# Kernel tuning notes

Measured on AMD Instinct MI355X. Metric: run time of the kernel, lower is better.

The kernel has to match this reference:

```python
import jax, jax.numpy as jnp
import numpy as np

V = 4          # view_num
B = 2048       # batch_size
D = 512        # feature dim
N = V * B
TEMP = 0.5     # temperature
EPS = 1e-8     # torch CosineSimilarity eps


def _neg_idx():
    # Row with residue p (position within its view block) masks out columns c
    # with c % B == p (the positive/self positions), exactly matching
    # mask_positive_samples: fill_diagonal_(0) on every BxB block.
    cols = np.arange(N)
    return np.stack([cols[cols % B != p] for p in range(B)])  # [B, N-V]

_NEG_IDX = jnp.asarray(_neg_idx())


def setup_inputs() -> dict:
    key = jax.random.key(0)
    x = jax.random.normal(key, (V, B, D), dtype=jnp.float32)
    return {"x": x}


def reference(x):
    # torch.cat(input, dim=0) -> [N, D]
    xf = x.reshape(N, D)
    # Cosine similarity via normalize + matmul (same math as broadcasted
    # CosineSimilarity(dim=2), expressed efficiently).
    norm = jnp.maximum(jnp.linalg.norm(xf, axis=1, keepdims=True), EPS)
    xn = xf / norm
    sim = (xn @ xn.T) / TEMP                                  # [N, N]

    # Negatives per anchor row: gather masked columns (same column order as
    # torch boolean-mask indexing, which is row-major ascending).
    sim_v = sim.reshape(V, B, N)
    negs = jnp.take_along_axis(sim_v, _NEG_IDX[None], axis=2)  # [V, B, N-V]
    lse_neg = jax.nn.logsumexp(negs, axis=2)                   # [V, B]

    # pos[i, j, b] = sim block-diagonal between views i and j
    pos = jnp.diagonal(sim.reshape(V, B, V, B), axis1=1, axis2=3)  # [V, V, B]

    # CrossEntropy with label 0 on logits = [pos_ij, negatives_i]:
    #   loss_b = logsumexp([pos, negs]) - pos = logaddexp(pos, lse_neg) - pos
    lse = jnp.logaddexp(pos, lse_neg[:, None, :])              # [V, V, B]
    per_pair = (lse - pos).sum(axis=2) / B                     # [V, V]

    off_diag = 1.0 - jnp.eye(V, dtype=per_pair.dtype)          # skip j == i
    return jnp.sum(per_pair * off_diag)
```

## Files before the change

kernel.cpp:

```cpp
#include <hip/hip_runtime.h>
#include <hip/hip_fp8.h>

#define NV 4
#define NB 2048
#define ND 512
#define NN 8192

typedef int int8v __attribute__((ext_vector_type(8)));
typedef int int4v __attribute__((ext_vector_type(4)));
typedef float floatx4 __attribute__((ext_vector_type(4)));
#define SCALE1 0x7F7F7F7Fu

__device__ __forceinline__ void lds_barrier() {
  asm volatile("s_waitcnt lgkmcnt(0)\n\ts_barrier" ::: "memory");
}

__global__ __launch_bounds__(256) void normalize_k(const float* __restrict__ x,
                                                   unsigned char* __restrict__ xn,
                                                   float* __restrict__ sumexp,
                                                   float* __restrict__ out) {
  if (threadIdx.x < 4) sumexp[blockIdx.x * 4 + threadIdx.x] = 0.0f;
  if (blockIdx.x == 0 && threadIdx.x == 0) out[0] = 0.0f;

  const int row = blockIdx.x * 4 + (threadIdx.x >> 6);
  const int l = threadIdx.x & 63;
  const float4* xr = (const float4*)(x + (size_t)row * ND);
  float4 v0 = xr[l * 2 + 0];
  float4 v1 = xr[l * 2 + 1];
  float ss = v0.x * v0.x + v0.y * v0.y + v0.z * v0.z + v0.w * v0.w +
             v1.x * v1.x + v1.y * v1.y + v1.z * v1.z + v1.w * v1.w;
#pragma unroll
  for (int off = 32; off > 0; off >>= 1) ss += __shfl_xor(ss, off, 64);
  const float inv = 1.0f / fmaxf(sqrtf(ss), 1e-8f);
  union { unsigned char b[8]; uint2 u; } pk;
  pk.b[0] = __hip_fp8_e4m3(v0.x * inv).__x;
  pk.b[1] = __hip_fp8_e4m3(v0.y * inv).__x;
  pk.b[2] = __hip_fp8_e4m3(v0.z * inv).__x;
  pk.b[3] = __hip_fp8_e4m3(v0.w * inv).__x;
  pk.b[4] = __hip_fp8_e4m3(v1.x * inv).__x;
  pk.b[5] = __hip_fp8_e4m3(v1.y * inv).__x;
  pk.b[6] = __hip_fp8_e4m3(v1.z * inv).__x;
  pk.b[7] = __hip_fp8_e4m3(v1.w * inv).__x;
  *(uint2*)(xn + (size_t)row * ND + l * 8) = pk.u;
}

__global__ __launch_bounds__(256) void sim_k(const unsigned char* __restrict__ xn,
                                             float* __restrict__ sumexp,
                                             float* __restrict__ pos) {
  __shared__ unsigned char As[128 * 128];
  __shared__ unsigned char Bs[128 * 128];
  const int tid = threadIdx.x;
  const int l = tid & 63;
  const int m = l & 15, q = l >> 4, s = l & 7;
  const int wr = (tid >> 6) >> 1, wc = (tid >> 6) & 1;

  const int bid = blockIdx.x;
  int rt = (int)((129.0f - sqrtf(16641.0f - 8.0f * (float)bid)) * 0.5f);
  rt = rt < 0 ? 0 : (rt > 63 ? 63 : rt);
  while (rt > 0 && (rt * 64 - rt * (rt - 1) / 2) > bid) --rt;
  while (rt < 63 && ((rt + 1) * 64 - (rt + 1) * rt / 2) <= bid) ++rt;
  const int ct = rt + (bid - (rt * 64 - rt * (rt - 1) / 2));
  const bool diag = (rt == ct);

  floatx4 acc[4][4] = {};

  const unsigned char* gA = xn + (size_t)rt * 128 * ND;
  const unsigned char* gB = xn + (size_t)ct * 128 * ND;

  const int crow = tid >> 3;
  const int coff = (tid & 7) * 16;
  const int lsw = ((tid & 7) ^ ((tid >> 3) & 7)) * 16;

  const int fo0 = ((2 * q + 0) ^ s) * 16;
  const int fo1 = ((2 * q + 1) ^ s) * 16;

  int4v pA[4], pB[4];
#pragma unroll
  for (int i = 0; i < 4; ++i) {
    const size_t go = (size_t)(i * 32 + crow) * ND + coff;
    pA[i] = *(const int4v*)(gA + go);
    pB[i] = *(const int4v*)(gB + go);
  }

#pragma unroll 1
  for (int kt = 0; kt < 4; ++kt) {
#pragma unroll
    for (int i = 0; i < 4; ++i) {
      const int la = (i * 32 + crow) * 128 + lsw;
      *(int4v*)(As + la) = pA[i];
      *(int4v*)(Bs + la) = pB[i];
    }
    lds_barrier();
    if (kt < 3) {
      const int kb = (kt + 1) * 128;
#pragma unroll
      for (int i = 0; i < 4; ++i) {
        const size_t go = (size_t)(i * 32 + crow) * ND + kb + coff;
        pA[i] = *(const int4v*)(gA + go);
        pB[i] = *(const int4v*)(gB + go);
      }
    }
    int8v af0, af1, af2, af3, bf0, bf1, bf2, bf3;
    {
      const unsigned char* pa0 = As + (wr * 64 + 0 * 16 + m) * 128;
      const unsigned char* pa1 = As + (wr * 64 + 1 * 16 + m) * 128;
      const unsigned char* pa2 = As + (wr * 64 + 2 * 16 + m) * 128;
      const unsigned char* pa3 = As + (wr * 64 + 3 * 16 + m) * 128;
      const unsigned char* pb0 = Bs + (wc * 64 + 0 * 16 + m) * 128;
      const unsigned char* pb1 = Bs + (wc * 64 + 1 * 16 + m) * 128;
      const unsigned char* pb2 = Bs + (wc * 64 + 2 * 16 + m) * 128;
      const unsigned char* pb3 = Bs + (wc * 64 + 3 * 16 + m) * 128;
      af0 = __builtin_shufflevector(*(const int4v*)(pa0 + fo0),
                                    *(const int4v*)(pa0 + fo1), 0,1,2,3,4,5,6,7);
      af1 = __builtin_shufflevector(*(const int4v*)(pa1 + fo0),
                                    *(const int4v*)(pa1 + fo1), 0,1,2,3,4,5,6,7);
      af2 = __builtin_shufflevector(*(const int4v*)(pa2 + fo0),
                                    *(const int4v*)(pa2 + fo1), 0,1,2,3,4,5,6,7);
      af3 = __builtin_shufflevector(*(const int4v*)(pa3 + fo0),
                                    *(const int4v*)(pa3 + fo1), 0,1,2,3,4,5,6,7);
      bf0 = __builtin_shufflevector(*(const int4v*)(pb0 + fo0),
                                    *(const int4v*)(pb0 + fo1), 0,1,2,3,4,5,6,7);
      bf1 = __builtin_shufflevector(*(const int4v*)(pb1 + fo0),
                                    *(const int4v*)(pb1 + fo1), 0,1,2,3,4,5,6,7);
      bf2 = __builtin_shufflevector(*(const int4v*)(pb2 + fo0),
                                    *(const int4v*)(pb2 + fo1), 0,1,2,3,4,5,6,7);
      bf3 = __builtin_shufflevector(*(const int4v*)(pb3 + fo0),
                                    *(const int4v*)(pb3 + fo1), 0,1,2,3,4,5,6,7);
    }
#define MFMA_ROW(mt, afv)                                                     \
  acc[mt][0] = __builtin_amdgcn_mfma_scale_f32_16x16x128_f8f6f4(              \
      afv, bf0, acc[mt][0], 0, 0, 0, SCALE1, 0, SCALE1);                      \
  acc[mt][1] = __builtin_amdgcn_mfma_scale_f32_16x16x128_f8f6f4(              \
      afv, bf1, acc[mt][1], 0, 0, 0, SCALE1, 0, SCALE1);                      \
  acc[mt][2] = __builtin_amdgcn_mfma_scale_f32_16x16x128_f8f6f4(              \
      afv, bf2, acc[mt][2], 0, 0, 0, SCALE1, 0, SCALE1);                      \
  acc[mt][3] = __builtin_amdgcn_mfma_scale_f32_16x16x128_f8f6f4(              \
      afv, bf3, acc[mt][3], 0, 0, 0, SCALE1, 0, SCALE1)
    MFMA_ROW(0, af0);
    MFMA_ROW(1, af1);
    MFMA_ROW(2, af2);
    MFMA_ROW(3, af3);
#undef MFMA_ROW
    lds_barrier();
  }

  const int r0 = rt * 128 + wr * 64;
  const int c0 = ct * 128 + wc * 64;
  float cs[4] = {0.f, 0.f, 0.f, 0.f};
#pragma unroll
  for (int mt = 0; mt < 4; ++mt) {
    float rs[4] = {0.f, 0.f, 0.f, 0.f};
#pragma unroll
    for (int nt = 0; nt < 4; ++nt) {
      const int c = c0 + nt * 16 + m;
#pragma unroll
      for (int reg = 0; reg < 4; ++reg) {
        const int r = r0 + mt * 16 + q * 4 + reg;
        const float sv = acc[mt][nt][reg] * 2.0f;
        if (((c - r) & (NB - 1)) == 0) {
          pos[r * NV + (c >> 11)] = sv;
          if (!diag) pos[c * NV + (r >> 11)] = sv;
        } else {
          const float e = __expf(sv);
          rs[reg] += e;
          cs[nt] += e;
        }
      }
    }
#pragma unroll
    for (int off = 1; off < 16; off <<= 1) {
#pragma unroll
      for (int reg = 0; reg < 4; ++reg) rs[reg] += __shfl_xor(rs[reg], off, 64);
    }
    if (m < 4) atomicAdd(&sumexp[r0 + mt * 16 + q * 4 + m], rs[m]);
  }
  if (!diag) {
#pragma unroll
    for (int nt = 0; nt < 4; ++nt) {
      cs[nt] += __shfl_xor(cs[nt], 16, 64);
      cs[nt] += __shfl_xor(cs[nt], 32, 64);
    }
    if (q == 0) {
#pragma unroll
      for (int nt = 0; nt < 4; ++nt)
        atomicAdd(&sumexp[c0 + nt * 16 + m], cs[nt]);
    }
  }
}

__global__ __launch_bounds__(256) void finalize_k(
    const float* __restrict__ sumexp, const float* __restrict__ pos,
    float* __restrict__ out) {
  const int r = blockIdx.x * 256 + threadIdx.x;
  const float se = sumexp[r];
  const int i = r >> 11;
  float local = 0.0f;
#pragma unroll
  for (int j = 0; j < NV; ++j) {
    if (j == i) continue;
    const float p = pos[r * NV + j];
    local += logf(__expf(p) + se) - p;
  }
  local *= (1.0f / NB);
#pragma unroll
  for (int off = 32; off > 0; off >>= 1) local += __shfl_xor(local, off, 64);
  if ((threadIdx.x & 63) == 0) atomicAdd(out, local);
}

extern "C" void kernel_launch(void* const* d_in, const int* in_sizes, int n_in,
                              void* d_out, int out_size, void* d_ws,
                              size_t ws_size, hipStream_t stream) {
  const float* x = (const float*)d_in[0];
  float* out = (float*)d_out;
  char* ws = (char*)d_ws;
  unsigned char* xn = (unsigned char*)ws;
  float* sumexp = (float*)(ws + (size_t)NN * ND);
  float* pos = (float*)(ws + (size_t)NN * ND + NN * 4);

  normalize_k<<<NN / 4, 256, 0, stream>>>(x, xn, sumexp, out);
  sim_k<<<64 * 65 / 2, 256, 0, stream>>>(xn, sumexp, pos);
  finalize_k<<<NN / 256, 256, 0, stream>>>(sumexp, pos, out);
}
```

Measured before the change: 110.5 us.

## Double-buffer LDS tiles in sim_k to drop one barrier per k-step

Doubles the shared-memory A and B tiles so the next k-slice is written into the alternate buffer while the current one is consumed. The global prefetch now runs two slices ahead, and each iteration needs one barrier instead of two. This raises LDS use to 64 KB per block, which may reduce how many blocks fit on a CU.

```diff
diff --git a/kernel.cpp b/kernel.cpp
--- a/kernel.cpp
+++ b/kernel.cpp
@@ -47,8 +47,8 @@
 __global__ __launch_bounds__(256) void sim_k(const unsigned char* __restrict__ xn,
                                              float* __restrict__ sumexp,
                                              float* __restrict__ pos) {
-  __shared__ unsigned char As[128 * 128];
-  __shared__ unsigned char Bs[128 * 128];
+  __shared__ unsigned char As[2][128 * 128];
+  __shared__ unsigned char Bs[2][128 * 128];
   const int tid = threadIdx.x;
   const int l = tid & 63;
   const int m = l & 15, q = l >> 4, s = l & 7;
@@ -70,6 +70,7 @@
   const int crow = tid >> 3;
   const int coff = (tid & 7) * 16;
   const int lsw = ((tid & 7) ^ ((tid >> 3) & 7)) * 16;
+  const int la = crow * 128 + lsw;
 
   const int fo0 = ((2 * q + 0) ^ s) * 16;
   const int fo1 = ((2 * q + 1) ^ s) * 16;
@@ -81,35 +82,33 @@
     pA[i] = *(const int4v*)(gA + go);
     pB[i] = *(const int4v*)(gB + go);
   }
+#pragma unroll
+  for (int i = 0; i < 4; ++i) {
+    *(int4v*)(&As[0][i * 4096 + la]) = pA[i];
+    *(int4v*)(&Bs[0][i * 4096 + la]) = pB[i];
+  }
+#pragma unroll
+  for (int i = 0; i < 4; ++i) {
+    const size_t go = (size_t)(i * 32 + crow) * ND + 128 + coff;
+    pA[i] = *(const int4v*)(gA + go);
+    pB[i] = *(const int4v*)(gB + go);
+  }
+  lds_barrier();
 
 #pragma unroll 1
   for (int kt = 0; kt < 4; ++kt) {
-#pragma unroll
-    for (int i = 0; i < 4; ++i) {
-      const int la = (i * 32 + crow) * 128 + lsw;
-      *(int4v*)(As + la) = pA[i];
-      *(int4v*)(Bs + la) = pB[i];
-    }
-    lds_barrier();
-    if (kt < 3) {
-      const int kb = (kt + 1) * 128;
-#pragma unroll
-      for (int i = 0; i < 4; ++i) {
-        const size_t go = (size_t)(i * 32 + crow) * ND + kb + coff;
-        pA[i] = *(const int4v*)(gA + go);
-        pB[i] = *(const int4v*)(gB + go);
-      }
-    }
+    const unsigned char* Ab = As[kt & 1];
+    const unsigned char* Bb = Bs[kt & 1];
     int8v af0, af1, af2, af3, bf0, bf1, bf2, bf3;
     {
-      const unsigned char* pa0 = As + (wr * 64 + 0 * 16 + m) * 128;
-      const unsigned char* pa1 = As + (wr * 64 + 1 * 16 + m) * 128;
-      const unsigned char* pa2 = As + (wr * 64 + 2 * 16 + m) * 128;
-      const unsigned char* pa3 = As + (wr * 64 + 3 * 16 + m) * 128;
-      const unsigned char* pb0 = Bs + (wc * 64 + 0 * 16 + m) * 128;
-      const unsigned char* pb1 = Bs + (wc * 64 + 1 * 16 + m) * 128;
-      const unsigned char* pb2 = Bs + (wc * 64 + 2 * 16 + m) * 128;
-      const unsigned char* pb3 = Bs + (wc * 64 + 3 * 16 + m) * 128;
+      const unsigned char* pa0 = Ab + (wr * 64 + 0 * 16 + m) * 128;
+      const unsigned char* pa1 = Ab + (wr * 64 + 1 * 16 + m) * 128;
+      const unsigned char* pa2 = Ab + (wr * 64 + 2 * 16 + m) * 128;
+      const unsigned char* pa3 = Ab + (wr * 64 + 3 * 16 + m) * 128;
+      const unsigned char* pb0 = Bb + (wc * 64 + 0 * 16 + m) * 128;
+      const unsigned char* pb1 = Bb + (wc * 64 + 1 * 16 + m) * 128;
+      const unsigned char* pb2 = Bb + (wc * 64 + 2 * 16 + m) * 128;
+      const unsigned char* pb3 = Bb + (wc * 64 + 3 * 16 + m) * 128;
       af0 = __builtin_shufflevector(*(const int4v*)(pa0 + fo0),
                                     *(const int4v*)(pa0 + fo1), 0,1,2,3,4,5,6,7);
       af1 = __builtin_shufflevector(*(const int4v*)(pa1 + fo0),
@@ -141,7 +140,25 @@
     MFMA_ROW(2, af2);
     MFMA_ROW(3, af3);
 #undef MFMA_ROW
-    lds_barrier();
+    if (kt < 3) {
+      unsigned char* An = As[(kt + 1) & 1];
+      unsigned char* Bn = Bs[(kt + 1) & 1];
+#pragma unroll
+      for (int i = 0; i < 4; ++i) {
+        *(int4v*)(&An[i * 4096 + la]) = pA[i];
+        *(int4v*)(&Bn[i * 4096 + la]) = pB[i];
+      }
+      if (kt < 2) {
+        const int kb = (kt + 2) * 128;
+#pragma unroll
+        for (int i = 0; i < 4; ++i) {
+          const size_t go = (size_t)(i * 32 + crow) * ND + kb + coff;
+          pA[i] = *(const int4v*)(gA + go);
+          pB[i] = *(const int4v*)(gB + go);
+        }
+      }
+      lds_barrier();
+    }
   }
 
   const int r0 = rt * 128 + wr * 64;
```

Result: no change. 111.8 us (+1.2%).
